# Performance work log

Hardware: AMD Instinct MI355X
Metric: run time of the kernel (lower is better)

Reference implementation:

```python
import jax, jax.numpy as jnp
import numpy as np

THR = 0.2          # config['thr']
BORDER = 2         # config['border_rm']
H0C, W0C = 60, 80  # coarse grid of image0 (L = 4800)
H1C, W1C = 60, 80  # coarse grid of image1 (S = 4800)
TEMP_INIT = 10.0


def _border_mask():
    # valid (non-border) positions of the [h0,w0,h1,w1] grid, flattened to [L,S]
    def ok(n):
        a = jnp.arange(n)
        return (a >= BORDER) & (a < n - BORDER)
    m = (ok(H0C)[:, None, None, None] & ok(W0C)[None, :, None, None]
         & ok(H1C)[None, None, :, None] & ok(W1C)[None, None, None, :])
    return m.reshape(H0C * W0C, H1C * W1C)


def setup_inputs() -> dict:
    key = jax.random.key(0)
    k0, k1 = jax.random.split(key)
    feat_c0 = jax.random.normal(k0, (2, 4800, 256), dtype=jnp.float32)
    feat_c1 = jax.random.normal(k1, (2, 4800, 256), dtype=jnp.float32)
    temperature = jnp.asarray(TEMP_INIT, dtype=jnp.float32)
    return {"feat_c0": feat_c0, "feat_c1": feat_c1, "temperature": temperature}


def reference(feat_c0, feat_c1, temperature):
    C = feat_c0.shape[-1]
    inv_sqrt_c = 1.0 / float(C) ** 0.5
    f0 = feat_c0 * inv_sqrt_c
    f1 = feat_c1 * inv_sqrt_c
    # dense similarity GEMM: [N,L,S]
    sim = jnp.einsum('nlc,nsc->nls', f0, f1) * temperature
    # dual softmax -> confidence matrix
    conf = jax.nn.softmax(sim, axis=1) * jax.nn.softmax(sim, axis=2)
    # threshold + border removal (mask_border with b=BORDER)
    mask = (conf > THR) & _border_mask()[None]
    # mutual nearest neighbor
    mutual = (mask
              & (conf == conf.max(axis=2, keepdims=True))
              & (conf == conf.max(axis=1, keepdims=True)))
    # dense mconf map: conf at selected matches, 0 elsewhere (fixed-shape
    # equivalent of the b_ids/i_ids/j_ids nonzero extraction)
    mconf = jnp.where(mutual, conf, jnp.zeros((), conf.dtype))
    return conf, mconf
```

## Files before the change

kernel.cpp:

```cpp
#include <hip/hip_runtime.h>
#include <hip/hip_bf16.h>

#define L 4800
#define CH 256
#define KS 768
#define NB 2
#define TT 38

typedef short short8 __attribute__((ext_vector_type(8)));
typedef float f32x4 __attribute__((ext_vector_type(4)));
typedef _Float16 h16;
typedef _Float16 h16x8 __attribute__((ext_vector_type(8)));

__device__ __forceinline__ unsigned short f2bf(float f) {
    unsigned u = __float_as_uint(f);
    unsigned r = (u + 0x7FFF + ((u >> 16) & 1)) >> 16;
    return (unsigned short)r;
}
__device__ __forceinline__ float bf2f(unsigned short h) {
    return __uint_as_float(((unsigned)h) << 16);
}

__global__ void init_stats(float* rowsum, float* colsum, unsigned* colmax, unsigned* cand_cnt) {
    int i = blockIdx.x * 256 + threadIdx.x;
    if (i < NB * L) { rowsum[i] = 0.f; colsum[i] = 0.f; colmax[i] = 0u; }
    if (i == 0) cand_cnt[0] = 0u;
}

__global__ void convert_kernel(const float* __restrict__ f0, const float* __restrict__ f1,
                               short* __restrict__ A, short* __restrict__ B) {
    int idx = blockIdx.x * 256 + threadIdx.x;
    if (idx >= NB * L * CH) return;
    int k = idx % CH;
    int r = (idx / CH) % L;
    int n = idx / (CH * L);
    long base = ((long)(n * L + r)) * KS;
    {
        float f = f0[idx];
        unsigned short h = f2bf(f);
        unsigned short lo = f2bf(f - bf2f(h));
        A[base + k]          = (short)h;
        A[base + CH + k]     = (short)h;
        A[base + 2 * CH + k] = (short)lo;
    }
    {
        float f = f1[idx];
        unsigned short h = f2bf(f);
        unsigned short lo = f2bf(f - bf2f(h));
        B[base + k]          = (short)h;
        B[base + CH + k]     = (short)lo;
        B[base + 2 * CH + k] = (short)h;
    }
}

__global__ __launch_bounds__(256) void gemm_exp(
    const short* __restrict__ A, const short* __restrict__ B,
    const float* __restrict__ temp,
    h16* __restrict__ E, float* __restrict__ rowsum, float* __restrict__ colsum)
{
    __shared__ __align__(16) short As[128 * 32];
    __shared__ __align__(16) short Bs[128 * 32];
    int bid = blockIdx.x;
    int n = bid / (TT * TT);
    int t = bid % (TT * TT);
    int tm = (t / TT) * 128;
    int tn = (t % TT) * 128;
    const short* Ab = A + (long)n * L * KS;
    const short* Bb = B + (long)n * L * KS;
    int tid = threadIdx.x;
    int lane = tid & 63;
    int w = tid >> 6;
    int wr = (w >> 1) * 64;
    int wc = (w & 1) * 64;

    f32x4 acc[4][4] = {};

    int lrow = lane >> 2;
    int kc8 = (lane & 3) * 8;

    for (int k0 = 0; k0 < KS; k0 += 32) {
        __syncthreads();
#pragma unroll
        for (int j = 0; j < 2; ++j) {
            int c = w * 2 + j;
            int row = c * 16 + lrow;
            int ga = tm + row; ga = ga > L - 1 ? L - 1 : ga;
            int gb = tn + row; gb = gb > L - 1 ? L - 1 : gb;
            __builtin_amdgcn_global_load_lds(
                (const __attribute__((address_space(1))) void*)(Ab + (long)ga * KS + k0 + kc8),
                (__attribute__((address_space(3))) void*)(As + c * 512), 16, 0, 0);
            __builtin_amdgcn_global_load_lds(
                (const __attribute__((address_space(1))) void*)(Bb + (long)gb * KS + k0 + kc8),
                (__attribute__((address_space(3))) void*)(Bs + c * 512), 16, 0, 0);
        }
        __syncthreads();

        short8 af[4], bf[4];
        int klo = (lane >> 4) * 8;
        int ra = wr + (lane & 15);
        int rb = wc + (lane & 15);
#pragma unroll
        for (int m = 0; m < 4; ++m) af[m] = *(const short8*)&As[(ra + m * 16) * 32 + klo];
#pragma unroll
        for (int nf = 0; nf < 4; ++nf) bf[nf] = *(const short8*)&Bs[(rb + nf * 16) * 32 + klo];
#pragma unroll
        for (int m = 0; m < 4; ++m)
#pragma unroll
            for (int nf = 0; nf < 4; ++nf)
                acc[m][nf] = __builtin_amdgcn_mfma_f32_16x16x32_bf16(af[m], bf[nf], acc[m][nf], 0, 0, 0);
    }

    float scale = temp[0] * (1.0f / 256.0f);
    float rpart[4][4];
#pragma unroll
    for (int m = 0; m < 4; ++m)
#pragma unroll
        for (int j = 0; j < 4; ++j) rpart[m][j] = 0.f;
    float cpart[4] = {0.f, 0.f, 0.f, 0.f};
    int row0 = tm + wr + ((lane >> 4) * 4);
    int col0 = tn + wc + (lane & 15);
#pragma unroll
    for (int m = 0; m < 4; ++m) {
#pragma unroll
        for (int nf = 0; nf < 4; ++nf) {
#pragma unroll
            for (int j = 0; j < 4; ++j) {
                int rr = row0 + m * 16 + j;
                int cc = col0 + nf * 16;
                float e = 0.f;
                if (rr < L && cc < L) {
                    e = __expf(acc[m][nf][j] * scale);
                    E[((long)n * L + rr) * L + cc] = (h16)e;
                }
                rpart[m][j] += e;
                cpart[nf] += e;
            }
        }
    }
#pragma unroll
    for (int m = 0; m < 4; ++m)
#pragma unroll
        for (int j = 0; j < 4; ++j) {
            float v = rpart[m][j];
            v += __shfl_xor(v, 1); v += __shfl_xor(v, 2);
            v += __shfl_xor(v, 4); v += __shfl_xor(v, 8);
            if ((lane & 15) == 0) {
                int rr = row0 + m * 16 + j;
                if (rr < L) atomicAdd(&rowsum[n * L + rr], v);
            }
        }
#pragma unroll
    for (int nf = 0; nf < 4; ++nf) {
        float v = cpart[nf];
        v += __shfl_xor(v, 16); v += __shfl_xor(v, 32);
        if ((lane >> 4) == 0) {
            int cc = col0 + nf * 16;
            if (cc < L) atomicAdd(&colsum[n * L + cc], v);
        }
    }
}

__global__ void inv_kernel(const float* rowsum, const float* colsum, float* inv_rs, float* inv_cs) {
    int i = blockIdx.x * 256 + threadIdx.x;
    if (i < NB * L) { inv_rs[i] = 1.0f / rowsum[i]; inv_cs[i] = 1.0f / colsum[i]; }
}

__global__ __launch_bounds__(256) void conf_row(
    const h16* __restrict__ E, const float* __restrict__ inv_rs, const float* __restrict__ inv_cs,
    float* __restrict__ conf, float* __restrict__ rowmax,
    unsigned* __restrict__ cand, unsigned* __restrict__ cand_cnt, unsigned cand_cap)
{
    int b = blockIdx.x;
    int n = b / L;
    const h16x8* E8 = (const h16x8*)(E + (long)b * L);
    const f32x4* IC4 = (const f32x4*)(inv_cs + n * L);
    float* Crow = conf + (long)b * L;
    float irs = inv_rs[b];
    int tid = threadIdx.x;
    float m = 0.f;
    for (int i = tid; i < L / 8; i += 256) {
        h16x8 e8 = E8[i];
        f32x4 ic0 = IC4[2 * i], ic1 = IC4[2 * i + 1];
        f32x4 c0, c1;
#pragma unroll
        for (int k = 0; k < 4; ++k) {
            float e = (float)e8[k];
            float tt = (e * e) * irs;
            c0[k] = tt * ic0[k];
            m = fmaxf(m, c0[k]);
        }
#pragma unroll
        for (int k = 0; k < 4; ++k) {
            float e = (float)e8[4 + k];
            float tt = (e * e) * irs;
            c1[k] = tt * ic1[k];
            m = fmaxf(m, c1[k]);
        }
        *(f32x4*)&Crow[i * 8] = c0;
        *(f32x4*)&Crow[i * 8 + 4] = c1;
#pragma unroll
        for (int k = 0; k < 4; ++k) {
            if (c0[k] > 0.2f) {
                unsigned pos = atomicAdd(cand_cnt, 1u);
                if (pos < cand_cap) cand[pos] = (unsigned)b * L + (unsigned)(i * 8 + k);
            }
            if (c1[k] > 0.2f) {
                unsigned pos = atomicAdd(cand_cnt, 1u);
                if (pos < cand_cap) cand[pos] = (unsigned)b * L + (unsigned)(i * 8 + 4 + k);
            }
        }
    }
#pragma unroll
    for (int off = 1; off < 64; off <<= 1) m = fmaxf(m, __shfl_xor(m, off));
    __shared__ float sm[4];
    int lane = tid & 63, wv = tid >> 6;
    if (lane == 0) sm[wv] = m;
    __syncthreads();
    if (tid == 0) rowmax[b] = fmaxf(fmaxf(sm[0], sm[1]), fmaxf(sm[2], sm[3]));
}

__global__ __launch_bounds__(256) void col_max(
    const h16* __restrict__ E, const float* __restrict__ inv_rs, const float* __restrict__ inv_cs,
    unsigned* __restrict__ colmax)
{
    int bx = blockIdx.x;
    int rc = bx & 31;
    int cc = (bx >> 5) % 19;
    int n = bx / (19 * 32);
    int col = cc * 256 + threadIdx.x;
    if (col >= L) return;
    const h16* p = E + ((long)n * L + rc * 150) * L + col;
    const float* irs = inv_rs + n * L + rc * 150;
    float m = 0.f;
    for (int i = 0; i < 150; ++i) {
        float e = (float)(*p);
        float tt = (e * e) * irs[i];
        m = fmaxf(m, tt);
        p += L;
    }
    float v = m * inv_cs[n * L + col];
    atomicMax(&colmax[n * L + col], __float_as_uint(v));
}

__global__ __launch_bounds__(256) void fill_zero(f32x4* __restrict__ p, long n4) {
    long i = (long)blockIdx.x * 256 + threadIdx.x;
    long stride = (long)gridDim.x * 256;
    f32x4 z = {0.f, 0.f, 0.f, 0.f};
    for (; i < n4; i += stride) p[i] = z;
}

__global__ __launch_bounds__(256) void cand_kernel(
    const unsigned* __restrict__ cand_cnt, const unsigned* __restrict__ cand, unsigned cand_cap,
    const float* __restrict__ conf, const float* __restrict__ rowmax,
    const unsigned* __restrict__ colmax, float* __restrict__ mconf)
{
    unsigned cnt = cand_cnt[0];
    if (cnt > cand_cap) cnt = cand_cap;
    for (unsigned i = blockIdx.x * 256 + threadIdx.x; i < cnt; i += gridDim.x * 256) {
        unsigned idx = cand[i];
        unsigned b = idx / L, s = idx % L;
        unsigned n = b / L, l = b % L;
        int h0 = l / 80, w0 = l % 80;
        int h1 = s / 80, w1 = s % 80;
        bool ok = (h0 >= 2) && (h0 < 58) && (w0 >= 2) && (w0 < 78)
               && (h1 >= 2) && (h1 < 58) && (w1 >= 2) && (w1 < 78);
        float c = conf[idx];
        if (ok && c == rowmax[b] && c == __uint_as_float(colmax[n * L + s]))
            mconf[idx] = c;
    }
}

extern "C" void kernel_launch(void* const* d_in, const int* in_sizes, int n_in,
                              void* d_out, int out_size, void* d_ws, size_t ws_size,
                              hipStream_t stream)
{
    const float* f0 = (const float*)d_in[0];
    const float* f1 = (const float*)d_in[1];
    const float* temp = (const float*)d_in[2];

    float* conf  = (float*)d_out;
    float* mconf = conf + (long)NB * L * L;
    h16*   E     = (h16*)mconf;

    short* Abf = (short*)d_out;
    short* Bbf = (short*)((char*)d_out + 32u * 1024u * 1024u);

    float* rowsum = (float*)d_ws;
    float* colsum = rowsum + NB * L;
    float* inv_rs = colsum + NB * L;
    float* inv_cs = inv_rs + NB * L;
    float* rowmax = inv_cs + NB * L;
    unsigned* colmax = (unsigned*)(rowmax + NB * L);
    unsigned* cand_cnt = colmax + NB * L;
    unsigned* cand = cand_cnt + 1;
    long stats_bytes = (char*)cand - (char*)d_ws;
    long cap_l = ((long)ws_size - stats_bytes) / 4;
    if (cap_l < 0) cap_l = 0;
    if (cap_l > (4 << 20)) cap_l = 4 << 20;
    unsigned cand_cap = (unsigned)cap_l;

    init_stats<<<(NB * L + 255) / 256, 256, 0, stream>>>(rowsum, colsum, colmax, cand_cnt);
    convert_kernel<<<(NB * L * CH + 255) / 256, 256, 0, stream>>>(f0, f1, Abf, Bbf);
    gemm_exp<<<NB * TT * TT, 256, 0, stream>>>(Abf, Bbf, temp, E, rowsum, colsum);
    inv_kernel<<<(NB * L + 255) / 256, 256, 0, stream>>>(rowsum, colsum, inv_rs, inv_cs);
    conf_row<<<NB * L, 256, 0, stream>>>(E, inv_rs, inv_cs, conf, rowmax, cand, cand_cnt, cand_cap);
    col_max<<<NB * 19 * 32, 256, 0, stream>>>(E, inv_rs, inv_cs, colmax);
    fill_zero<<<2048, 256, 0, stream>>>((f32x4*)mconf, (long)NB * L * L / 4);
    cand_kernel<<<128, 256, 0, stream>>>(cand_cnt, cand, cand_cap, conf, rowmax, colmax, mconf);
}
```

Baseline: 540.5 us.

## Use single-pass fp16 GEMM, fuse init into convert, and fold mconf zeroing into conf_row

Drops the three-term split-bf16 emulation, which tripled the K dimension, in favour of one fp16 MFMA pass over K=256. This cuts GEMM work and conversion traffic to about a third. The stats init is merged into a vectorised conversion kernel. When the workspace is large enough, the exp buffer moves into it so conf_row can zero mconf and the separate fill pass is skipped. The cost is lower GEMM precision (fp16 inputs), which may flip threshold or argmax decisions near ties, and the candidate capacity is now fixed.

Result: no change. 531.8 us (-1.6%).

```diff
diff --git a/kernel.cpp b/kernel.cpp
--- a/kernel.cpp
+++ b/kernel.cpp
@@ -1,72 +1,48 @@
 #include <hip/hip_runtime.h>
-#include <hip/hip_bf16.h>
 
 #define L 4800
 #define CH 256
-#define KS 768
 #define NB 2
 #define TT 38
 
-typedef short short8 __attribute__((ext_vector_type(8)));
 typedef float f32x4 __attribute__((ext_vector_type(4)));
 typedef _Float16 h16;
+typedef _Float16 h16x4 __attribute__((ext_vector_type(4)));
 typedef _Float16 h16x8 __attribute__((ext_vector_type(8)));
 
-__device__ __forceinline__ unsigned short f2bf(float f) {
-    unsigned u = __float_as_uint(f);
-    unsigned r = (u + 0x7FFF + ((u >> 16) & 1)) >> 16;
-    return (unsigned short)r;
-}
-__device__ __forceinline__ float bf2f(unsigned short h) {
-    return __uint_as_float(((unsigned)h) << 16);
-}
-
-__global__ void init_stats(float* rowsum, float* colsum, unsigned* colmax, unsigned* cand_cnt) {
-    int i = blockIdx.x * 256 + threadIdx.x;
-    if (i < NB * L) { rowsum[i] = 0.f; colsum[i] = 0.f; colmax[i] = 0u; }
-    if (i == 0) cand_cnt[0] = 0u;
-}
-
-__global__ void convert_kernel(const float* __restrict__ f0, const float* __restrict__ f1,
-                               short* __restrict__ A, short* __restrict__ B) {
+__global__ __launch_bounds__(256) void convert_init(
+    const float* __restrict__ f0, const float* __restrict__ f1,
+    h16* __restrict__ A, h16* __restrict__ B,
+    float* __restrict__ rowsum, float* __restrict__ colsum,
+    unsigned* __restrict__ colmax, unsigned* __restrict__ cand_cnt)
+{
     int idx = blockIdx.x * 256 + threadIdx.x;
-    if (idx >= NB * L * CH) return;
-    int k = idx % CH;
-    int r = (idx / CH) % L;
-    int n = idx / (CH * L);
-    long base = ((long)(n * L + r)) * KS;
-    {
-        float f = f0[idx];
-        unsigned short h = f2bf(f);
-        unsigned short lo = f2bf(f - bf2f(h));
-        A[base + k]          = (short)h;
-        A[base + CH + k]     = (short)h;
-        A[base + 2 * CH + k] = (short)lo;
-    }
-    {
-        float f = f1[idx];
-        unsigned short h = f2bf(f);
-        unsigned short lo = f2bf(f - bf2f(h));
-        B[base + k]          = (short)h;
-        B[base + CH + k]     = (short)lo;
-        B[base + 2 * CH + k] = (short)h;
-    }
+    if (idx < NB * L) { rowsum[idx] = 0.f; colsum[idx] = 0.f; colmax[idx] = 0u; }
+    if (idx == 0) cand_cnt[0] = 0u;
+    if (idx >= NB * L * CH / 4) return;
+    f32x4 a = ((const f32x4*)f0)[idx];
+    f32x4 b = ((const f32x4*)f1)[idx];
+    h16x4 ah, bh;
+#pragma unroll
+    for (int k = 0; k < 4; ++k) { ah[k] = (h16)a[k]; bh[k] = (h16)b[k]; }
+    ((h16x4*)A)[idx] = ah;
+    ((h16x4*)B)[idx] = bh;
 }
 
 __global__ __launch_bounds__(256) void gemm_exp(
-    const short* __restrict__ A, const short* __restrict__ B,
+    const h16* __restrict__ A, const h16* __restrict__ B,
     const float* __restrict__ temp,
     h16* __restrict__ E, float* __restrict__ rowsum, float* __restrict__ colsum)
 {
-    __shared__ __align__(16) short As[128 * 32];
-    __shared__ __align__(16) short Bs[128 * 32];
+    __shared__ __align__(16) h16 As[128 * 32];
+    __shared__ __align__(16) h16 Bs[128 * 32];
     int bid = blockIdx.x;
     int n = bid / (TT * TT);
     int t = bid % (TT * TT);
     int tm = (t / TT) * 128;
     int tn = (t % TT) * 128;
-    const short* Ab = A + (long)n * L * KS;
-    const short* Bb = B + (long)n * L * KS;
+    const h16* Ab = A + (long)n * L * CH;
+    const h16* Bb = B + (long)n * L * CH;
     int tid = threadIdx.x;
     int lane = tid & 63;
     int w = tid >> 6;
@@ -78,7 +54,7 @@
     int lrow = lane >> 2;
     int kc8 = (lane & 3) * 8;
 
-    for (int k0 = 0; k0 < KS; k0 += 32) {
+    for (int k0 = 0; k0 < CH; k0 += 32) {
         __syncthreads();
 #pragma unroll
         for (int j = 0; j < 2; ++j) {
@@ -87,27 +63,27 @@
             int ga = tm + row; ga = ga > L - 1 ? L - 1 : ga;
             int gb = tn + row; gb = gb > L - 1 ? L - 1 : gb;
             __builtin_amdgcn_global_load_lds(
-                (const __attribute__((address_space(1))) void*)(Ab + (long)ga * KS + k0 + kc8),
+                (const __attribute__((address_space(1))) void*)(Ab + (long)ga * CH + k0 + kc8),
                 (__attribute__((address_space(3))) void*)(As + c * 512), 16, 0, 0);
             __builtin_amdgcn_global_load_lds(
-                (const __attribute__((address_space(1))) void*)(Bb + (long)gb * KS + k0 + kc8),
+                (const __attribute__((address_space(1))) void*)(Bb + (long)gb * CH + k0 + kc8),
                 (__attribute__((address_space(3))) void*)(Bs + c * 512), 16, 0, 0);
         }
         __syncthreads();
 
-        short8 af[4], bf[4];
+        h16x8 af[4], bf[4];
         int klo = (lane >> 4) * 8;
         int ra = wr + (lane & 15);
         int rb = wc + (lane & 15);
 #pragma unroll
-        for (int m = 0; m < 4; ++m) af[m] = *(const short8*)&As[(ra + m * 16) * 32 + klo];
-#pragma unroll
-        for (int nf = 0; nf < 4; ++nf) bf[nf] = *(const short8*)&Bs[(rb + nf * 16) * 32 + klo];
+        for (int m = 0; m < 4; ++m) af[m] = *(const h16x8*)&As[(ra + m * 16) * 32 + klo];
+#pragma unroll
+        for (int nf = 0; nf < 4; ++nf) bf[nf] = *(const h16x8*)&Bs[(rb + nf * 16) * 32 + klo];
 #pragma unroll
         for (int m = 0; m < 4; ++m)
 #pragma unroll
             for (int nf = 0; nf < 4; ++nf)
-                acc[m][nf] = __builtin_amdgcn_mfma_f32_16x16x32_bf16(af[m], bf[nf], acc[m][nf], 0, 0, 0);
+                acc[m][nf] = __builtin_amdgcn_mfma_f32_16x16x32_f16(af[m], bf[nf], acc[m][nf], 0, 0, 0);
     }
 
     float scale = temp[0] * (1.0f / 256.0f);
@@ -168,6 +144,7 @@
 __global__ __launch_bounds__(256) void conf_row(
     const h16* __restrict__ E, const float* __restrict__ inv_rs, const float* __restrict__ inv_cs,
     float* __restrict__ conf, float* __restrict__ rowmax,
+    float* __restrict__ mzero,
     unsigned* __restrict__ cand, unsigned* __restrict__ cand_cnt, unsigned cand_cap)
 {
     int b = blockIdx.x;
@@ -209,6 +186,11 @@
                 if (pos < cand_cap) cand[pos] = (unsigned)b * L + (unsigned)(i * 8 + 4 + k);
             }
         }
+    }
+    if (mzero) {
+        f32x4* M4 = (f32x4*)(mzero + (long)b * L);
+        f32x4 z = {0.f, 0.f, 0.f, 0.f};
+        for (int i = tid; i < L / 4; i += 256) M4[i] = z;
     }
 #pragma unroll
     for (int off = 1; off < 64; off <<= 1) m = fmaxf(m, __shfl_xor(m, off));
@@ -280,10 +262,9 @@
 
     float* conf  = (float*)d_out;
     float* mconf = conf + (long)NB * L * L;
-    h16*   E     = (h16*)mconf;
-
-    short* Abf = (short*)d_out;
-    short* Bbf = (short*)((char*)d_out + 32u * 1024u * 1024u);
+
+    h16* Abf = (h16*)d_out;
+    h16* Bbf = (h16*)((char*)d_out + 8u * 1024u * 1024u);
 
     float* rowsum = (float*)d_ws;
     float* colsum = rowsum + NB * L;
@@ -293,18 +274,22 @@
     unsigned* colmax = (unsigned*)(rowmax + NB * L);
     unsigned* cand_cnt = colmax + NB * L;
     unsigned* cand = cand_cnt + 1;
-    long stats_bytes = (char*)cand - (char*)d_ws;
-    long cap_l = ((long)ws_size - stats_bytes) / 4;
-    if (cap_l < 0) cap_l = 0;
-    if (cap_l > (4 << 20)) cap_l = 4 << 20;
-    unsigned cand_cap = (unsigned)cap_l;
-
-    init_stats<<<(NB * L + 255) / 256, 256, 0, stream>>>(rowsum, colsum, colmax, cand_cnt);
-    convert_kernel<<<(NB * L * CH + 255) / 256, 256, 0, stream>>>(f0, f1, Abf, Bbf);
+    const unsigned cand_cap = 1u << 20;
+    size_t stats_end = (size_t)((char*)(cand + cand_cap) - (char*)d_ws);
+    size_t E_off = (stats_end + 255) & ~(size_t)255;
+    size_t E_bytes = (size_t)NB * L * L * 2;
+    bool E_in_ws = ws_size >= E_off + E_bytes;
+    h16* E = E_in_ws ? (h16*)((char*)d_ws + E_off) : (h16*)mconf;
+
+    convert_init<<<(NB * L * CH / 4 + 255) / 256, 256, 0, stream>>>(
+        f0, f1, Abf, Bbf, rowsum, colsum, colmax, cand_cnt);
     gemm_exp<<<NB * TT * TT, 256, 0, stream>>>(Abf, Bbf, temp, E, rowsum, colsum);
     inv_kernel<<<(NB * L + 255) / 256, 256, 0, stream>>>(rowsum, colsum, inv_rs, inv_cs);
-    conf_row<<<NB * L, 256, 0, stream>>>(E, inv_rs, inv_cs, conf, rowmax, cand, cand_cnt, cand_cap);
+    conf_row<<<NB * L, 256, 0, stream>>>(E, inv_rs, inv_cs, conf, rowmax,
+                                         E_in_ws ? mconf : (float*)nullptr,
+                                         cand, cand_cnt, cand_cap);
     col_max<<<NB * 19 * 32, 256, 0, stream>>>(E, inv_rs, inv_cs, colmax);
-    fill_zero<<<2048, 256, 0, stream>>>((f32x4*)mconf, (long)NB * L * L / 4);
+    if (!E_in_ws)
+        fill_zero<<<2048, 256, 0, stream>>>((f32x4*)mconf, (long)NB * L * L / 4);
     cand_kernel<<<128, 256, 0, stream>>>(cand_cnt, cand, cand_cap, conf, rowmax, colmax, mconf);
 }
```
